# Kernel optimization log

Measured on AMD Instinct MI355X. Metric: run time of the kernel, lower is better.

The kernel has to match this reference:

```python
import jax, jax.numpy as jnp
import numpy as np

H, DK, DV, SEG, D = 16, 64, 64, 512, 1024


def setup_inputs() -> dict:
    key = jax.random.key(0)
    ks = jax.random.split(key, 6)
    B, T = 2, 8192
    x = jax.random.normal(ks[0], (B, T, D), jnp.float32)
    Wq = jax.random.normal(ks[1], (H * DK, D), jnp.float32) * 0.02
    Wk = jax.random.normal(ks[2], (H * DK, D), jnp.float32) * 0.02
    Wv = jax.random.normal(ks[3], (H * DV, D), jnp.float32) * 0.02
    Wout = jax.random.normal(ks[4], (D, H * DV), jnp.float32) * 0.02
    betas = jax.random.normal(ks[5], (1, H, 1, DV), jnp.float32)
    return {"x": x, "Wq": Wq, "Wk": Wk, "Wv": Wv, "Wout": Wout, "betas": betas}


def reference(x, Wq, Wk, Wv, Wout, betas):
    B, T, _ = x.shape
    n_seg = T // SEG
    # Projections for the whole sequence, then PyTorch-style .view head split:
    # per segment, (B, SEG, H*dk).view(B, H, SEG, dk) is a raw row-major reshape.
    q = (x @ Wq.T).reshape(B, n_seg, H, SEG, DK)
    k = (x @ Wk.T).reshape(B, n_seg, H, SEG, DK)
    v = (x @ Wv.T).reshape(B, n_seg, H, SEG, DV)
    qs = jnp.moveaxis(q, 1, 0)  # (n_seg, B, H, SEG, DK)
    ks_ = jnp.moveaxis(k, 1, 0)
    vs = jnp.moveaxis(v, 1, 0)

    gate = jax.nn.sigmoid(betas)                 # (1, H, 1, DV)
    scale = 1.0 / jnp.sqrt(jnp.float32(DK))

    mem0 = jnp.zeros((B, H, DK, DV), x.dtype)
    # z broadcasts from (B,H,DV,1) to (B,H,DV,DK) on first update; start dense.
    z0 = jnp.zeros((B, H, DV, DK), x.dtype)

    def step(carry, seg):
        mem, z = carry
        q, k, v = seg
        sq = jax.nn.elu(q) + 1.0                 # (B,H,S,DK)
        sk = jax.nn.elu(k) + 1.0
        z = z + sk.sum(axis=-2, keepdims=True)   # (B,H,DV,DK) via broadcast
        scores = jnp.einsum('bhsd,bhtd->bhst', q, k) * scale
        att_dot = jnp.einsum('bhst,bhtv->bhsv', jax.nn.softmax(scores, axis=-1), v)
        att_mem = jnp.einsum('bhsd,bhdv->bhsv', sq, mem) / jnp.einsum('bhsd,bhdv->bhsv', sq, z)
        mem = mem + jnp.einsum('bhsd,bhsv->bhdv', sk, v)  # linear update (after att_mem)
        att = gate * att_mem + (1.0 - gate) * att_dot     # (B,H,S,DV)
        # PyTorch .view(B, SEG, H*DV) on (B,H,S,DV): raw reshape, no transpose.
        y = att.reshape(B, SEG, H * DV) @ Wout.T          # (B,SEG,D)
        return (mem, z), y

    (_, _), ys = jax.lax.scan(step, (mem0, z0), (qs, ks_, vs))
    out = jnp.moveaxis(ys, 0, 1).reshape(B, T, D)
    return out
```

## Files before the change

### kernel.cpp

```cpp
#include <hip/hip_runtime.h>


#define H_ 16
#define SEG_ 512
#define NSEG_ 16
#define B_ 2
#define T_ 8192
#define D_ 1024
#define BT_ 16384

#define NPROJ ((size_t)BT_ * D_)
#define NW ((size_t)D_ * D_)

__device__ unsigned short g_qb[NPROJ], g_kb[NPROJ], g_vb[NPROJ];
__device__ unsigned short g_xh[NPROJ];
__device__ unsigned short g_wqkv[3 * NW];
__device__ unsigned short g_ath[NPROJ], g_atl[NPROJ];
__device__ unsigned short g_woh[NW], g_wol[NW];
__device__ unsigned short g_vt[(size_t)512 * 64 * 512];
__device__ float g_M[(size_t)512 * 4096];
__device__ float g_z[(size_t)512 * 64];

typedef __attribute__((ext_vector_type(8))) short short8;
typedef __attribute__((ext_vector_type(8))) unsigned short ushort8;
typedef __attribute__((ext_vector_type(4))) float f32x4;

__device__ __forceinline__ float elu1(float x) {
    return x > 0.f ? x + 1.f : __expf(x);
}
__device__ __forceinline__ unsigned short f2bf(float x) {
    unsigned u = __float_as_uint(x);
    u += 0x7fffu + ((u >> 16) & 1u);
    return (unsigned short)(u >> 16);
}
__device__ __forceinline__ float bf2f(unsigned short h) {
    return __uint_as_float((unsigned)h << 16);
}
__device__ __forceinline__ void load_lds16(const unsigned short* g, unsigned short* l) {
    __builtin_amdgcn_global_load_lds(
        (const __attribute__((address_space(1))) unsigned int*)g,
        (__attribute__((address_space(3))) unsigned int*)l, 16, 0, 0);
}

__global__ __launch_bounds__(256) void cast_bf16(
    const float* __restrict__ in, unsigned short* __restrict__ out, int n)
{
    int i = (blockIdx.x * 256 + threadIdx.x) * 4;
    if (i >= n) return;
    float4 x = *(const float4*)(in + i);
    ushort4 h;
    h.x = f2bf(x.x); h.y = f2bf(x.y); h.z = f2bf(x.z); h.w = f2bf(x.w);
    *(ushort4*)(out + i) = h;
}

__global__ __launch_bounds__(256) void split_bf16(
    const float* __restrict__ in, unsigned short* __restrict__ hi,
    unsigned short* __restrict__ lo, int n)
{
    int i = (blockIdx.x * 256 + threadIdx.x) * 4;
    if (i >= n) return;
    float4 x = *(const float4*)(in + i);
    ushort4 h, l;
    h.x = f2bf(x.x); l.x = f2bf(x.x - bf2f(h.x));
    h.y = f2bf(x.y); l.y = f2bf(x.y - bf2f(h.y));
    h.z = f2bf(x.z); l.z = f2bf(x.z - bf2f(h.z));
    h.w = f2bf(x.w); l.w = f2bf(x.w - bf2f(h.w));
    *(ushort4*)(hi + i) = h;
    *(ushort4*)(lo + i) = l;
}


#define VMC(N) asm volatile("s_waitcnt vmcnt(" #N ")" ::: "memory")

#define STAGE_A(p, h, tt, u) \
    load_lds16(Aw + ((h) * 128 + (u) * 8) * 1024 + (tt) * 64, \
               &lds[(p) * 32768 + ((h) * 128 + w * 16 + (u) * 8) * 64])
#define STAGE_B(p, h, tt, u) \
    load_lds16(Bww + ((h) * 128 + (u) * 8) * 1024 + (tt) * 64, \
               &lds[(p) * 32768 + 16384 + ((h) * 128 + w * 16 + (u) * 8) * 64])
#define STAGE_AH(p, h, tt) do { STAGE_A(p, h, tt, 0); STAGE_A(p, h, tt, 1); } while (0)
#define STAGE_BH(p, h, tt) do { STAGE_B(p, h, tt, 0); STAGE_B(p, h, tt, 1); } while (0)

#define LDA(PBUF, MLO) do { \
    _Pragma("unroll") for (int m2 = 0; m2 < 4; ++m2) \
    _Pragma("unroll") for (int ks2 = 0; ks2 < 2; ++ks2) \
        a[m2][ks2] = *(const short8*)&lds[(PBUF) * 32768 + aoff[ks2] + ((MLO) + m2) * 1024]; \
} while (0)

#define LDB(PBUF) do { \
    _Pragma("unroll") for (int n2 = 0; n2 < 4; ++n2) \
    _Pragma("unroll") for (int ks2 = 0; ks2 < 2; ++ks2) \
        b[n2][ks2] = *(const short8*)&lds[(PBUF) * 32768 + boff[ks2] + n2 * 1024]; \
} while (0)

#define MFMA_QUAD(MLO, NLO) do { \
    _Pragma("unroll") for (int m2 = 0; m2 < 4; ++m2) \
    _Pragma("unroll") for (int n2 = 0; n2 < 2; ++n2) \
    _Pragma("unroll") for (int ks2 = 0; ks2 < 2; ++ks2) \
        acc[(MLO) + m2][(NLO) + n2] = __builtin_amdgcn_mfma_f32_16x16x32_bf16( \
            a[m2][ks2], b[(NLO) + n2][ks2], acc[(MLO) + m2][(NLO) + n2], 0, 0, 0); \
} while (0)

#define PH(MLO, NLO) do { \
    __builtin_amdgcn_s_barrier(); \
    asm volatile("s_waitcnt lgkmcnt(0)" ::: "memory"); \
    __builtin_amdgcn_sched_barrier(0); \
    __builtin_amdgcn_s_setprio(1); \
    MFMA_QUAD(MLO, NLO); \
    __builtin_amdgcn_s_setprio(0); \
    __builtin_amdgcn_sched_barrier(0); \
    __builtin_amdgcn_s_barrier(); \
} while (0)

__global__ __launch_bounds__(512, 2) void gemm_qkv8(
    const unsigned short* __restrict__ A, const unsigned short* __restrict__ Bw,
    unsigned short* __restrict__ Q, unsigned short* __restrict__ Kp,
    unsigned short* __restrict__ V)
{
    __shared__ unsigned short lds[65536];
    const int t = threadIdx.x, lane = t & 63, w = t >> 6;
    const int wave_m = w >> 2, wave_n = w & 3;

    const int bid = blockIdx.x;
    const int sb = (bid & 7) * 96 + (bid >> 3);
    const int mb = sb / 12, nb = sb % 12;
    const int m0 = mb * 256, n0 = nb * 256;

    const int lrow = lane >> 3;
    const int lcol = ((lane & 7) ^ lrow) * 8;
    const unsigned short* Aw  = A  + (size_t)(m0 + w * 16 + lrow) * 1024 + lcol;
    const unsigned short* Bww = Bw + (size_t)(n0 + w * 16 + lrow) * 1024 + lcol;

    const int fr = lane & 15, g4 = lane >> 4;
    int aoff[2], boff[2];
#pragma unroll
    for (int ks2 = 0; ks2 < 2; ++ks2) {
        aoff[ks2] = (wave_m * 128 + fr) * 64 + (((ks2 * 4 + g4) ^ (fr & 7)) * 8);
        boff[ks2] = 16384 + (wave_n * 64 + fr) * 64 + (((ks2 * 4 + g4) ^ (fr & 7)) * 8);
    }

    f32x4 acc[8][4];
#pragma unroll
    for (int i = 0; i < 8; ++i)
#pragma unroll
        for (int j = 0; j < 4; ++j) acc[i][j] = (f32x4)0.f;
    short8 a[4][2], b[4][2];

    STAGE_BH(0, 0, 0); STAGE_BH(0, 1, 0); STAGE_AH(0, 0, 0); STAGE_AH(0, 1, 0);
    STAGE_BH(1, 0, 1); STAGE_BH(1, 1, 1); STAGE_AH(1, 0, 1);
    VMC(6);
    __builtin_amdgcn_s_barrier();

#pragma unroll 1
    for (int it = 0; it < 7; ++it) {
        const int t1 = 2 * it + 1, t2 = 2 * it + 2, t3 = 2 * it + 3;
        LDB(0); LDA(0, 0);
        STAGE_AH(1, 1, t1);
        PH(0, 0);
        STAGE_BH(0, 0, t2);
        PH(0, 2);
        LDA(0, 4);
        STAGE_BH(0, 1, t2);
        PH(4, 0);
        STAGE_AH(0, 0, t2);
        VMC(6);
        PH(4, 2);
        LDB(1); LDA(1, 0);
        STAGE_AH(0, 1, t2);
        PH(0, 0);
        STAGE_BH(1, 0, t3);
        PH(0, 2);
        LDA(1, 4);
        STAGE_BH(1, 1, t3);
        PH(4, 0);
        STAGE_AH(1, 0, t3);
        VMC(6);
        PH(4, 2);
    }
    LDB(0); LDA(0, 0);
    STAGE_AH(1, 1, 15);
    PH(0, 0);
    PH(0, 2);
    LDA(0, 4);
    PH(4, 0);
    VMC(0);
    PH(4, 2);
    LDB(1); LDA(1, 0);
    PH(0, 0);
    PH(0, 2);
    LDA(1, 4);
    PH(4, 0);
    PH(4, 2);

    const int ccol = lane & 15, crow = (lane >> 4) * 4;
#pragma unroll
    for (int m = 0; m < 8; ++m)
#pragma unroll
        for (int n = 0; n < 4; ++n) {
            const int row = wave_m * 128 + m * 16 + crow;
            const int col = wave_n * 64 + n * 16 + ccol;
#pragma unroll
            for (int r = 0; r < 4; ++r)
                lds[(row + r) * 256 + col] = f2bf(acc[m][n][r]);
        }
    __syncthreads();
    const int which = n0 >> 10, col0 = n0 & 1023;
    unsigned short* outp = which == 0 ? Q : (which == 1 ? Kp : V);
    const int orow = t >> 1, och = (t & 1) * 128;
    unsigned short* gp = outp + (size_t)(m0 + orow) * 1024 + col0 + och;
    const unsigned short* lp = &lds[orow * 256 + och];
#pragma unroll
    for (int u = 0; u < 128; u += 8)
        *(ushort8*)(gp + u) = *(const ushort8*)(lp + u);
}


#define OSTG(p, arrp, aroff, tt, u) \
    load_lds16(arrp + (size_t)(u) * 16 * 1024 + (tt) * 32, \
               &lds[(p) * 32768 + (aroff) + (w * 32 + (u) * 16) * 32])
#define OUNIT(p, arrp, aroff, tt) do { OSTG(p, arrp, aroff, tt, 0); OSTG(p, arrp, aroff, tt, 1); } while (0)

#define OLDA(PBUF, MLO) do { \
    _Pragma("unroll") for (int m2 = 0; m2 < 4; ++m2) { \
        ah[m2] = *(const short8*)&lds[(PBUF) * 32768 +         ao + ((MLO) + m2) * 512]; \
        al[m2] = *(const short8*)&lds[(PBUF) * 32768 +  8192 + ao + ((MLO) + m2) * 512]; \
    } \
} while (0)

#define OLDB(PBUF) do { \
    _Pragma("unroll") for (int n2 = 0; n2 < 4; ++n2) { \
        bh[n2] = *(const short8*)&lds[(PBUF) * 32768 + 16384 + bo + n2 * 512]; \
        bl[n2] = *(const short8*)&lds[(PBUF) * 32768 + 24576 + bo + n2 * 512]; \
    } \
} while (0)

#define OQUAD(MLO, NLO) do { \
    _Pragma("unroll") for (int m2 = 0; m2 < 4; ++m2) \
    _Pragma("unroll") for (int n2 = 0; n2 < 2; ++n2) { \
        acc[(MLO) + m2][(NLO) + n2] = __builtin_amdgcn_mfma_f32_16x16x32_bf16( \
            ah[m2], bh[(NLO) + n2], acc[(MLO) + m2][(NLO) + n2], 0, 0, 0); \
        acc[(MLO) + m2][(NLO) + n2] = __builtin_amdgcn_mfma_f32_16x16x32_bf16( \
            al[m2], bh[(NLO) + n2], acc[(MLO) + m2][(NLO) + n2], 0, 0, 0); \
        acc[(MLO) + m2][(NLO) + n2] = __builtin_amdgcn_mfma_f32_16x16x32_bf16( \
            ah[m2], bl[(NLO) + n2], acc[(MLO) + m2][(NLO) + n2], 0, 0, 0); \
    } \
} while (0)

#define OPH(MLO, NLO) do { \
    __builtin_amdgcn_s_barrier(); \
    asm volatile("s_waitcnt lgkmcnt(0)" ::: "memory"); \
    __builtin_amdgcn_sched_barrier(0); \
    __builtin_amdgcn_s_setprio(1); \
    OQUAD(MLO, NLO); \
    __builtin_amdgcn_s_setprio(0); \
    __builtin_amdgcn_sched_barrier(0); \
    __builtin_amdgcn_s_barrier(); \
} while (0)

__global__ __launch_bounds__(512, 2) void gemm_bt8(
    const unsigned short* __restrict__ Ah, const unsigned short* __restrict__ Al,
    const unsigned short* __restrict__ Bh, const unsigned short* __restrict__ Bl,
    float* __restrict__ C)
{
    __shared__ unsigned short lds[65536];
    const int t = threadIdx.x, lane = t & 63, w = t >> 6;
    const int wave_m = w >> 2, wave_n = w & 3;

    const int bid = blockIdx.x;
    const int sb = (bid & 7) * 32 + (bid >> 3);
    const int m0 = (sb >> 2) * 256, n0 = (sb & 3) * 256;

    const int lrow = lane >> 2;
    const int lcol = ((lane & 3) ^ ((lane >> 3) & 3)) * 8;
    const unsigned short* Ahp = Ah + (size_t)(m0 + w * 32 + lrow) * 1024 + lcol;
    const unsigned short* Alp = Al + (size_t)(m0 + w * 32 + lrow) * 1024 + lcol;
    const unsigned short* Bhp = Bh + (size_t)(n0 + w * 32 + lrow) * 1024 + lcol;
    const unsigned short* Blp = Bl + (size_t)(n0 + w * 32 + lrow) * 1024 + lcol;

    const int fr = lane & 15, g4 = lane >> 4;
    const int xo = (g4 ^ ((fr >> 1) & 3)) * 8;
    const int ao = (wave_m * 128 + fr) * 32 + xo;
    const int bo = (wave_n * 64 + fr) * 32 + xo;

    f32x4 acc[8][4];
#pragma unroll
    for (int i = 0; i < 8; ++i)
#pragma unroll
        for (int j = 0; j < 4; ++j) acc[i][j] = (f32x4)0.f;
    short8 ah[4], al[4], bh[4], bl[4];

    OUNIT(0, Bhp, 16384, 0); OUNIT(0, Blp, 24576, 0); OUNIT(0, Ahp, 0, 0); OUNIT(0, Alp, 8192, 0);
    OUNIT(1, Bhp, 16384, 1); OUNIT(1, Blp, 24576, 1); OUNIT(1, Ahp, 0, 1);
    VMC(6);
    __builtin_amdgcn_s_barrier();

#pragma unroll 1
    for (int it = 0; it < 15; ++it) {
        const int t1 = 2 * it + 1, t2 = 2 * it + 2, t3 = 2 * it + 3;
        OLDB(0); OLDA(0, 0);
        OUNIT(1, Alp, 8192, t1);
        OPH(0, 0);
        OUNIT(0, Bhp, 16384, t2);
        OPH(0, 2);
        OLDA(0, 4);
        OUNIT(0, Blp, 24576, t2);
        OPH(4, 0);
        OUNIT(0, Ahp, 0, t2);
        VMC(6);
        OPH(4, 2);
        OLDB(1); OLDA(1, 0);
        OUNIT(0, Alp, 8192, t2);
        OPH(0, 0);
        OUNIT(1, Bhp, 16384, t3);
        OPH(0, 2);
        OLDA(1, 4);
        OUNIT(1, Blp, 24576, t3);
        OPH(4, 0);
        OUNIT(1, Ahp, 0, t3);
        VMC(6);
        OPH(4, 2);
    }
    OLDB(0); OLDA(0, 0);
    OUNIT(1, Alp, 8192, 31);
    OPH(0, 0);
    OPH(0, 2);
    OLDA(0, 4);
    OPH(4, 0);
    VMC(0);
    OPH(4, 2);
    OLDB(1); OLDA(1, 0);
    OPH(0, 0);
    OPH(0, 2);
    OLDA(1, 4);
    OPH(4, 0);
    OPH(4, 2);

    const int ccol = lane & 15, crow = (lane >> 4) * 4;
#pragma unroll
    for (int m = 0; m < 8; ++m)
#pragma unroll
        for (int n = 0; n < 4; ++n) {
            float* cp = C + (size_t)(m0 + wave_m * 128 + m * 16 + crow) * 1024
                          + (n0 + wave_n * 64 + n * 16 + ccol);
#pragma unroll
            for (int r = 0; r < 4; ++r) cp[(size_t)r * 1024] = acc[m][n][r];
        }
}

__global__ __launch_bounds__(256) void seg_stats(
    const unsigned short* __restrict__ kproj, const unsigned short* __restrict__ vproj,
    float* __restrict__ Mseg, float* __restrict__ zsum,
    unsigned short* __restrict__ vtg)
{
    __shared__ float ks[64][68];
    __shared__ float vs[64][68];
    const int idx = blockIdx.x;
    const int seg = idx & 15;
    const int bh  = idx >> 4;
    const int h   = bh & 15;
    const int b   = bh >> 4;
    const size_t base = ((size_t)b * T_ + (size_t)seg * SEG_ + (size_t)h * 32) * D_;
    const unsigned short* kt = kproj + base;
    const unsigned short* vt = vproj + base;
    const int t  = threadIdx.x;
    const int d0 = (t >> 4) * 4;
    const int v0 = (t & 15) * 4;
    const int lr = t >> 2;
    const int lc = (t & 3) * 16;
    float acc[4][4];
#pragma unroll
    for (int i = 0; i < 4; ++i)
#pragma unroll
        for (int j = 0; j < 4; ++j) acc[i][j] = 0.f;
    float zacc = 0.f;

    for (int c0 = 0; c0 < SEG_; c0 += 64) {
        __syncthreads();
        {
            const unsigned short* kp = kt + (size_t)(c0 + lr) * 64 + lc;
            const unsigned short* vp = vt + (size_t)(c0 + lr) * 64 + lc;
            ushort8 k0 = *(const ushort8*)kp,       k1 = *(const ushort8*)(kp + 8);
            ushort8 v0v = *(const ushort8*)vp,      v1 = *(const ushort8*)(vp + 8);
#pragma unroll
            for (int e = 0; e < 8; ++e) {
                ks[lr][lc + e]     = elu1(bf2f(k0[e]));
                ks[lr][lc + 8 + e] = elu1(bf2f(k1[e]));
                vs[lr][lc + e]     = bf2f(v0v[e]);
                vs[lr][lc + 8 + e] = bf2f(v1[e]);
            }
        }
        __syncthreads();
#pragma unroll 8
        for (int i = 0; i < 64; ++i) {
            float a0 = ks[i][d0 + 0], a1 = ks[i][d0 + 1];
            float a2 = ks[i][d0 + 2], a3 = ks[i][d0 + 3];
            float b0 = vs[i][v0 + 0], b1 = vs[i][v0 + 1];
            float b2 = vs[i][v0 + 2], b3 = vs[i][v0 + 3];
            acc[0][0] += a0 * b0; acc[0][1] += a0 * b1; acc[0][2] += a0 * b2; acc[0][3] += a0 * b3;
            acc[1][0] += a1 * b0; acc[1][1] += a1 * b1; acc[1][2] += a1 * b2; acc[1][3] += a1 * b3;
            acc[2][0] += a2 * b0; acc[2][1] += a2 * b1; acc[2][2] += a2 * b2; acc[2][3] += a2 * b3;
            acc[3][0] += a3 * b0; acc[3][1] += a3 * b1; acc[3][2] += a3 * b2; acc[3][3] += a3 * b3;
        }
        if (t < 64) {
#pragma unroll 8
            for (int i = 0; i < 64; ++i) zacc += ks[i][t];
        }
        {
            ushort8 w0, w1;
#pragma unroll
            for (int i = 0; i < 8; ++i) w0[i] = f2bf(vs[lc + i][lr]);
#pragma unroll
            for (int i = 0; i < 8; ++i) w1[i] = f2bf(vs[lc + 8 + i][lr]);
            unsigned short* vo = vtg + ((size_t)idx * 64 + lr) * 512 + c0 + lc;
            *(ushort8*)vo       = w0;
            *(ushort8*)(vo + 8) = w1;
        }
    }
    float* Mout = Mseg + (size_t)idx * 4096;
#pragma unroll
    for (int i = 0; i < 4; ++i)
        *(float4*)(Mout + (size_t)(d0 + i) * 64 + v0) =
            make_float4(acc[i][0], acc[i][1], acc[i][2], acc[i][3]);
    if (t < 64) zsum[(size_t)idx * 64 + t] = zacc;
}

__global__ __launch_bounds__(256) void prefix_scan(
    float* __restrict__ M, float* __restrict__ z)
{
    const int bh = blockIdx.x;
    const int t  = threadIdx.x;
    float run[16];
#pragma unroll
    for (int u = 0; u < 16; ++u) run[u] = 0.f;
    float runz = 0.f;
    for (int seg = 0; seg < NSEG_; ++seg) {
        const size_t o = ((size_t)bh * NSEG_ + seg) * 4096 + (size_t)t * 16;
#pragma unroll
        for (int u = 0; u < 16; u += 4) {
            float4 m = *(const float4*)(M + o + u);
            *(float4*)(M + o + u) = make_float4(run[u], run[u+1], run[u+2], run[u+3]);
            run[u] += m.x; run[u+1] += m.y; run[u+2] += m.z; run[u+3] += m.w;
        }
        if (t < 64) {
            const size_t oz = ((size_t)bh * NSEG_ + seg) * 64 + t;
            runz += z[oz];
            z[oz] = runz;
        }
    }
}

__global__ __launch_bounds__(256) void attn_mfma(
    const unsigned short* __restrict__ qproj, const unsigned short* __restrict__ kproj,
    const unsigned short* __restrict__ vtg, const float* __restrict__ memb,
    const float* __restrict__ Zaf, const float* __restrict__ betas,
    unsigned short* __restrict__ ath, unsigned short* __restrict__ atl)
{
    __shared__ unsigned short sm_k[64 * 72];
    __shared__ unsigned short sm_v[64 * 72];
    __shared__ unsigned short sm_p[64 * 72];
    __shared__ float Zsh[64], gsh[64];

    const int idx  = blockIdx.x;
    const int qc   = idx & 7;
    const int rest = idx >> 3;
    const int seg  = rest & 15;
    const int bh   = rest >> 4;
    const int h    = bh & 15;
    const int b    = bh >> 4;
    const size_t base = ((size_t)b * T_ + (size_t)seg * SEG_ + (size_t)h * 32) * D_;

    const int t    = threadIdx.x;
    const int lane = t & 63;
    const int w    = t >> 6;
    const int c16  = lane & 15;
    const int g4   = lane >> 4;
    const int lr   = t >> 2;
    const int lc   = (t & 3) * 16;

    const unsigned short* qt = qproj + base + (size_t)qc * 4096;
    const unsigned short* kt = kproj + base;
    const unsigned short* vt = vtg + (size_t)rest * (64 * 512);
    const float* mb = memb + (size_t)rest * 4096;

    if (t < 64) {
        Zsh[t] = Zaf[(size_t)rest * 64 + t];
        gsh[t] = 1.f / (1.f + __expf(-betas[h * 64 + t]));
    }

    short8 qh[2], sqh[2];
    float rowsum = 0.f;
#pragma unroll
    for (int ks = 0; ks < 2; ++ks) {
        const unsigned short* qp = qt + (size_t)(w * 16 + c16) * 64 + g4 * 8 + ks * 32;
        ushort8 qv = *(const ushort8*)qp;
        short8 qf, sf;
#pragma unroll
        for (int j = 0; j < 8; ++j) {
            float e = elu1(bf2f(qv[j]));
            rowsum += e;
            qf[j] = (short)qv[j];
            sf[j] = (short)f2bf(e);
        }
        qh[ks] = qf; sqh[ks] = sf;
    }
    rowsum += __shfl_xor(rowsum, 16);
    rowsum += __shfl_xor(rowsum, 32);

    {
        const float* mp = mb + (size_t)lr * 64 + lc;
#pragma unroll
        for (int u = 0; u < 4; ++u) {
            float4 m4 = *(const float4*)(mp + u * 4);
            sm_p[(lc + u * 4 + 0) * 72 + lr] = f2bf(m4.x);
            sm_p[(lc + u * 4 + 1) * 72 + lr] = f2bf(m4.y);
            sm_p[(lc + u * 4 + 2) * 72 + lr] = f2bf(m4.z);
            sm_p[(lc + u * 4 + 3) * 72 + lr] = f2bf(m4.w);
        }
    }
    __syncthreads();

    f32x4 numf[4];
#pragma unroll
    for (int nf = 0; nf < 4; ++nf) numf[nf] = (f32x4)0.f;
#pragma unroll
    for (int ks = 0; ks < 2; ++ks)
#pragma unroll
        for (int nf = 0; nf < 4; ++nf) {
            short8 bm = *(const short8*)&sm_p[(nf * 16 + c16) * 72 + g4 * 8 + ks * 32];
            numf[nf] = __builtin_amdgcn_mfma_f32_16x16x32_bf16(sqh[ks], bm, numf[nf], 0, 0, 0);
        }

    f32x4 o[4];
#pragma unroll
    for (int nf = 0; nf < 4; ++nf) o[nf] = (f32x4)0.f;
    float mrow[4] = {-1e30f, -1e30f, -1e30f, -1e30f};
    float lrow[4] = {0.f, 0.f, 0.f, 0.f};

    for (int kb = 0; kb < 8; ++kb) {
        __syncthreads();
        {
            const unsigned short* kp = kt + (size_t)(kb * 64 + lr) * 64 + lc;
            *(ushort8*)&sm_k[lr * 72 + lc]     = *(const ushort8*)kp;
            *(ushort8*)&sm_k[lr * 72 + lc + 8] = *(const ushort8*)(kp + 8);
            const unsigned short* vp = vt + (size_t)lr * 512 + kb * 64 + lc;
            *(ushort8*)&sm_v[lr * 72 + lc]     = *(const ushort8*)vp;
            *(ushort8*)&sm_v[lr * 72 + lc + 8] = *(const ushort8*)(vp + 8);
        }
        __syncthreads();

        f32x4 s[4];
#pragma unroll
        for (int nf = 0; nf < 4; ++nf) s[nf] = (f32x4)0.f;
#pragma unroll
        for (int ks = 0; ks < 2; ++ks)
#pragma unroll
            for (int nf = 0; nf < 4; ++nf) {
                short8 bk = *(const short8*)&sm_k[(nf * 16 + c16) * 72 + g4 * 8 + ks * 32];
                s[nf] = __builtin_amdgcn_mfma_f32_16x16x32_bf16(qh[ks], bk, s[nf], 0, 0, 0);
            }
#pragma unroll
        for (int nf = 0; nf < 4; ++nf) s[nf] *= 0.125f;

        float corr[4];
#pragma unroll
        for (int r = 0; r < 4; ++r) {
            float mx = fmaxf(fmaxf(s[0][r], s[1][r]), fmaxf(s[2][r], s[3][r]));
            mx = fmaxf(mx, __shfl_xor(mx, 1));
            mx = fmaxf(mx, __shfl_xor(mx, 2));
            mx = fmaxf(mx, __shfl_xor(mx, 4));
            mx = fmaxf(mx, __shfl_xor(mx, 8));
            float mnew = fmaxf(mrow[r], mx);
            corr[r] = __expf(mrow[r] - mnew);
            mrow[r] = mnew;
        }
#pragma unroll
        for (int nf = 0; nf < 4; ++nf)
#pragma unroll
            for (int r = 0; r < 4; ++r)
                s[nf][r] = __expf(s[nf][r] - mrow[r]);
#pragma unroll
        for (int r = 0; r < 4; ++r) {
            float ps = s[0][r] + s[1][r] + s[2][r] + s[3][r];
            ps += __shfl_xor(ps, 1);
            ps += __shfl_xor(ps, 2);
            ps += __shfl_xor(ps, 4);
            ps += __shfl_xor(ps, 8);
            lrow[r] = lrow[r] * corr[r] + ps;
        }
#pragma unroll
        for (int nf = 0; nf < 4; ++nf)
#pragma unroll
            for (int r = 0; r < 4; ++r) o[nf][r] *= corr[r];

#pragma unroll
        for (int nf = 0; nf < 4; ++nf)
#pragma unroll
            for (int r = 0; r < 4; ++r)
                sm_p[(w * 16 + g4 * 4 + r) * 72 + nf * 16 + c16] = f2bf(s[nf][r]);

#pragma unroll
        for (int ks = 0; ks < 2; ++ks) {
            short8 pa = *(const short8*)&sm_p[(w * 16 + c16) * 72 + g4 * 8 + ks * 32];
#pragma unroll
            for (int nf = 0; nf < 4; ++nf) {
                short8 bv = *(const short8*)&sm_v[(nf * 16 + c16) * 72 + g4 * 8 + ks * 32];
                o[nf] = __builtin_amdgcn_mfma_f32_16x16x32_bf16(pa, bv, o[nf], 0, 0, 0);
            }
        }
    }

    __syncthreads();

    float rs[4], invl[4];
#pragma unroll
    for (int r = 0; r < 4; ++r) {
        rs[r]   = __shfl(rowsum, (g4 << 2) + r);
        invl[r] = 1.f / lrow[r];
    }
#pragma unroll
    for (int nf = 0; nf < 4; ++nf) {
        const int col = nf * 16 + c16;
        const float Zc = Zsh[col], gc = gsh[col];
        const float izc = 1.f / Zc;
#pragma unroll
        for (int r = 0; r < 4; ++r) {
            const float adot = o[nf][r] * invl[r];
            const float amem = numf[nf][r] * izc / rs[r];
            const float res  = gc * amem + (1.f - gc) * adot;
            const unsigned short hv = f2bf(res);
            const unsigned short lv = f2bf(res - bf2f(hv));
            const int row = w * 16 + g4 * 4 + r;
            sm_k[row * 72 + col] = hv;
            sm_v[row * 72 + col] = lv;
        }
    }
    __syncthreads();
    {
        const size_t ob = base + (size_t)(qc * 64 + lr) * 64 + lc;
        *(ushort8*)(ath + ob)     = *(const ushort8*)&sm_k[lr * 72 + lc];
        *(ushort8*)(ath + ob + 8) = *(const ushort8*)&sm_k[lr * 72 + lc + 8];
        *(ushort8*)(atl + ob)     = *(const ushort8*)&sm_v[lr * 72 + lc];
        *(ushort8*)(atl + ob + 8) = *(const ushort8*)&sm_v[lr * 72 + lc + 8];
    }
}

extern "C" void kernel_launch(void* const* d_in, const int* in_sizes, int n_in,
                              void* d_out, int out_size, void* d_ws, size_t ws_size,
                              hipStream_t stream) {
    const float* x     = (const float*)d_in[0];
    const float* Wq    = (const float*)d_in[1];
    const float* Wk    = (const float*)d_in[2];
    const float* Wv    = (const float*)d_in[3];
    const float* Wout  = (const float*)d_in[4];
    const float* betas = (const float*)d_in[5];
    float* out = (float*)d_out;
    (void)d_ws; (void)ws_size;

    float *M, *z;
    unsigned short *qb, *kb, *vb, *xh, *wqkv, *vt, *ath, *atl, *woh, *wol;
    hipGetSymbolAddress((void**)&qb,   HIP_SYMBOL(g_qb));
    hipGetSymbolAddress((void**)&kb,   HIP_SYMBOL(g_kb));
    hipGetSymbolAddress((void**)&vb,   HIP_SYMBOL(g_vb));
    hipGetSymbolAddress((void**)&xh,   HIP_SYMBOL(g_xh));
    hipGetSymbolAddress((void**)&wqkv, HIP_SYMBOL(g_wqkv));
    hipGetSymbolAddress((void**)&vt,   HIP_SYMBOL(g_vt));
    hipGetSymbolAddress((void**)&ath,  HIP_SYMBOL(g_ath));
    hipGetSymbolAddress((void**)&atl,  HIP_SYMBOL(g_atl));
    hipGetSymbolAddress((void**)&woh,  HIP_SYMBOL(g_woh));
    hipGetSymbolAddress((void**)&wol,  HIP_SYMBOL(g_wol));
    hipGetSymbolAddress((void**)&M,    HIP_SYMBOL(g_M));
    hipGetSymbolAddress((void**)&z,    HIP_SYMBOL(g_z));

    const int nX = (int)NPROJ, nW = (int)NW;
    cast_bf16<<<nX / 1024, 256, 0, stream>>>(x, xh, nX);
    cast_bf16<<<nW / 1024, 256, 0, stream>>>(Wq, wqkv, nW);
    cast_bf16<<<nW / 1024, 256, 0, stream>>>(Wk, wqkv + NW, nW);
    cast_bf16<<<nW / 1024, 256, 0, stream>>>(Wv, wqkv + 2 * NW, nW);
    split_bf16<<<nW / 1024, 256, 0, stream>>>(Wout, woh, wol, nW);

    gemm_qkv8<<<dim3(768), 512, 0, stream>>>(xh, wqkv, qb, kb, vb);
    seg_stats<<<B_ * H_ * NSEG_, 256, 0, stream>>>(kb, vb, M, z, vt);
    prefix_scan<<<B_ * H_, 256, 0, stream>>>(M, z);
    attn_mfma<<<B_ * H_ * NSEG_ * 8, 256, 0, stream>>>(qb, kb, vt, M, z, betas, ath, atl);
    gemm_bt8<<<dim3(256), 512, 0, stream>>>(ath, atl, woh, wol, out);
}
```

Measured before the change: 559.6 us.

## Swizzle attention LDS tiles, lazy softmax rescale, MFMA row sums, remap blocks

Replaces the padded 72-stride LDS tiles in the attention kernel with an XOR-swizzled 64-stride layout to avoid bank conflicts while using less shared memory. The online softmax now rescales only when some row max exceeds the running max by more than 8, skipping the shuffle reductions and output rescaling in most iterations. Row sums of P are computed with an extra MFMA against a ones vector instead of shuffles. The block index mapping is also reordered so neighbouring blocks share different (b,h,seg) tiles. The lazy threshold relies on exp staying bounded in fp32/bf16.

```diff
diff --git a/kernel.cpp b/kernel.cpp
--- a/kernel.cpp
+++ b/kernel.cpp
@@ -40,6 +40,9 @@
     __builtin_amdgcn_global_load_lds(
         (const __attribute__((address_space(1))) unsigned int*)g,
         (__attribute__((address_space(3))) unsigned int*)l, 16, 0, 0);
+}
+__device__ __forceinline__ int sz8(int row, int blk) {
+    return row * 64 + ((blk ^ (row & 7)) << 3);
 }
 
 __global__ __launch_bounds__(256) void cast_bf16(
@@ -455,16 +458,16 @@
     const float* __restrict__ Zaf, const float* __restrict__ betas,
     unsigned short* __restrict__ ath, unsigned short* __restrict__ atl)
 {
-    __shared__ unsigned short sm_k[64 * 72];
-    __shared__ unsigned short sm_v[64 * 72];
-    __shared__ unsigned short sm_p[64 * 72];
+    __shared__ unsigned short sm_k[64 * 64];
+    __shared__ unsigned short sm_v[64 * 64];
+    __shared__ unsigned short sm_p[64 * 64];
     __shared__ float Zsh[64], gsh[64];
 
     const int idx  = blockIdx.x;
-    const int qc   = idx & 7;
-    const int rest = idx >> 3;
+    const int qc   = (idx >> 3) & 7;
+    const int rest = (idx >> 6) * 8 + (idx & 7);
+    const int bh   = rest >> 4;
     const int seg  = rest & 15;
-    const int bh   = rest >> 4;
     const int h    = bh & 15;
     const int b    = bh >> 4;
     const size_t base = ((size_t)b * T_ + (size_t)seg * SEG_ + (size_t)h * 32) * D_;
@@ -511,10 +514,10 @@
 #pragma unroll
         for (int u = 0; u < 4; ++u) {
             float4 m4 = *(const float4*)(mp + u * 4);
-            sm_p[(lc + u * 4 + 0) * 72 + lr] = f2bf(m4.x);
-            sm_p[(lc + u * 4 + 1) * 72 + lr] = f2bf(m4.y);
-            sm_p[(lc + u * 4 + 2) * 72 + lr] = f2bf(m4.z);
-            sm_p[(lc + u * 4 + 3) * 72 + lr] = f2bf(m4.w);
+            sm_p[sz8(lc + u * 4 + 0, lr >> 3) + (lr & 7)] = f2bf(m4.x);
+            sm_p[sz8(lc + u * 4 + 1, lr >> 3) + (lr & 7)] = f2bf(m4.y);
+            sm_p[sz8(lc + u * 4 + 2, lr >> 3) + (lr & 7)] = f2bf(m4.z);
+            sm_p[sz8(lc + u * 4 + 3, lr >> 3) + (lr & 7)] = f2bf(m4.w);
         }
     }
     __syncthreads();
@@ -526,9 +529,13 @@
     for (int ks = 0; ks < 2; ++ks)
 #pragma unroll
         for (int nf = 0; nf < 4; ++nf) {
-            short8 bm = *(const short8*)&sm_p[(nf * 16 + c16) * 72 + g4 * 8 + ks * 32];
+            short8 bm = *(const short8*)&sm_p[sz8(nf * 16 + c16, g4 + ks * 4)];
             numf[nf] = __builtin_amdgcn_mfma_f32_16x16x32_bf16(sqh[ks], bm, numf[nf], 0, 0, 0);
         }
+
+    short8 bones;
+#pragma unroll
+    for (int j = 0; j < 8; ++j) bones[j] = (short)0x3F80;
 
     f32x4 o[4];
 #pragma unroll
@@ -540,11 +547,11 @@
         __syncthreads();
         {
             const unsigned short* kp = kt + (size_t)(kb * 64 + lr) * 64 + lc;
-            *(ushort8*)&sm_k[lr * 72 + lc]     = *(const ushort8*)kp;
-            *(ushort8*)&sm_k[lr * 72 + lc + 8] = *(const ushort8*)(kp + 8);
+            *(ushort8*)&sm_k[sz8(lr, lc >> 3)]       = *(const ushort8*)kp;
+            *(ushort8*)&sm_k[sz8(lr, (lc >> 3) + 1)] = *(const ushort8*)(kp + 8);
             const unsigned short* vp = vt + (size_t)lr * 512 + kb * 64 + lc;
-            *(ushort8*)&sm_v[lr * 72 + lc]     = *(const ushort8*)vp;
-            *(ushort8*)&sm_v[lr * 72 + lc + 8] = *(const ushort8*)(vp + 8);
+            *(ushort8*)&sm_v[sz8(lr, lc >> 3)]       = *(const ushort8*)vp;
+            *(ushort8*)&sm_v[sz8(lr, (lc >> 3) + 1)] = *(const ushort8*)(vp + 8);
         }
         __syncthreads();
 
@@ -555,58 +562,56 @@
         for (int ks = 0; ks < 2; ++ks)
 #pragma unroll
             for (int nf = 0; nf < 4; ++nf) {
-                short8 bk = *(const short8*)&sm_k[(nf * 16 + c16) * 72 + g4 * 8 + ks * 32];
+                short8 bk = *(const short8*)&sm_k[sz8(nf * 16 + c16, g4 + ks * 4)];
                 s[nf] = __builtin_amdgcn_mfma_f32_16x16x32_bf16(qh[ks], bk, s[nf], 0, 0, 0);
             }
 #pragma unroll
         for (int nf = 0; nf < 4; ++nf) s[nf] *= 0.125f;
 
-        float corr[4];
-#pragma unroll
-        for (int r = 0; r < 4; ++r) {
-            float mx = fmaxf(fmaxf(s[0][r], s[1][r]), fmaxf(s[2][r], s[3][r]));
-            mx = fmaxf(mx, __shfl_xor(mx, 1));
-            mx = fmaxf(mx, __shfl_xor(mx, 2));
-            mx = fmaxf(mx, __shfl_xor(mx, 4));
-            mx = fmaxf(mx, __shfl_xor(mx, 8));
-            float mnew = fmaxf(mrow[r], mx);
-            corr[r] = __expf(mrow[r] - mnew);
-            mrow[r] = mnew;
+        float pmax[4];
+#pragma unroll
+        for (int r = 0; r < 4; ++r)
+            pmax[r] = fmaxf(fmaxf(s[0][r], s[1][r]), fmaxf(s[2][r], s[3][r]));
+        const bool ok = pmax[0] <= mrow[0] + 8.f && pmax[1] <= mrow[1] + 8.f &&
+                        pmax[2] <= mrow[2] + 8.f && pmax[3] <= mrow[3] + 8.f;
+        if (!__all(ok)) {
+#pragma unroll
+            for (int r = 0; r < 4; ++r) {
+                float mx = pmax[r];
+                mx = fmaxf(mx, __shfl_xor(mx, 1));
+                mx = fmaxf(mx, __shfl_xor(mx, 2));
+                mx = fmaxf(mx, __shfl_xor(mx, 4));
+                mx = fmaxf(mx, __shfl_xor(mx, 8));
+                const float mnew = fmaxf(mrow[r], mx);
+                const float corr = __expf(mrow[r] - mnew);
+                mrow[r] = mnew;
+                lrow[r] *= corr;
+#pragma unroll
+                for (int nf = 0; nf < 4; ++nf) o[nf][r] *= corr;
+            }
         }
 #pragma unroll
         for (int nf = 0; nf < 4; ++nf)
 #pragma unroll
-            for (int r = 0; r < 4; ++r)
+            for (int r = 0; r < 4; ++r) {
                 s[nf][r] = __expf(s[nf][r] - mrow[r]);
-#pragma unroll
-        for (int r = 0; r < 4; ++r) {
-            float ps = s[0][r] + s[1][r] + s[2][r] + s[3][r];
-            ps += __shfl_xor(ps, 1);
-            ps += __shfl_xor(ps, 2);
-            ps += __shfl_xor(ps, 4);
-            ps += __shfl_xor(ps, 8);
-            lrow[r] = lrow[r] * corr[r] + ps;
-        }
-#pragma unroll
-        for (int nf = 0; nf < 4; ++nf)
-#pragma unroll
-            for (int r = 0; r < 4; ++r) o[nf][r] *= corr[r];
-
-#pragma unroll
-        for (int nf = 0; nf < 4; ++nf)
-#pragma unroll
-            for (int r = 0; r < 4; ++r)
-                sm_p[(w * 16 + g4 * 4 + r) * 72 + nf * 16 + c16] = f2bf(s[nf][r]);
-
+                sm_p[sz8(w * 16 + g4 * 4 + r, nf * 2 + (c16 >> 3)) + (c16 & 7)] =
+                    f2bf(s[nf][r]);
+            }
+
+        f32x4 psum = (f32x4)0.f;
 #pragma unroll
         for (int ks = 0; ks < 2; ++ks) {
-            short8 pa = *(const short8*)&sm_p[(w * 16 + c16) * 72 + g4 * 8 + ks * 32];
+            short8 pa = *(const short8*)&sm_p[sz8(w * 16 + c16, g4 + ks * 4)];
+            psum = __builtin_amdgcn_mfma_f32_16x16x32_bf16(pa, bones, psum, 0, 0, 0);
 #pragma unroll
             for (int nf = 0; nf < 4; ++nf) {
-                short8 bv = *(const short8*)&sm_v[(nf * 16 + c16) * 72 + g4 * 8 + ks * 32];
+                short8 bv = *(const short8*)&sm_v[sz8(nf * 16 + c16, g4 + ks * 4)];
                 o[nf] = __builtin_amdgcn_mfma_f32_16x16x32_bf16(pa, bv, o[nf], 0, 0, 0);
             }
         }
+#pragma unroll
+        for (int r = 0; r < 4; ++r) lrow[r] += psum[r];
     }
 
     __syncthreads();
@@ -630,17 +635,18 @@
             const unsigned short hv = f2bf(res);
             const unsigned short lv = f2bf(res - bf2f(hv));
             const int row = w * 16 + g4 * 4 + r;
-            sm_k[row * 72 + col] = hv;
-            sm_v[row * 72 + col] = lv;
+            const int so  = sz8(row, nf * 2 + (c16 >> 3)) + (c16 & 7);
+            sm_k[so] = hv;
+            sm_v[so] = lv;
         }
     }
     __syncthreads();
     {
         const size_t ob = base + (size_t)(qc * 64 + lr) * 64 + lc;
-        *(ushort8*)(ath + ob)     = *(const ushort8*)&sm_k[lr * 72 + lc];
-        *(ushort8*)(ath + ob + 8) = *(const ushort8*)&sm_k[lr * 72 + lc + 8];
-        *(ushort8*)(atl + ob)     = *(const ushort8*)&sm_v[lr * 72 + lc];
-        *(ushort8*)(atl + ob + 8) = *(const ushort8*)&sm_v[lr * 72 + lc + 8];
+        *(ushort8*)(ath + ob)     = *(const ushort8*)&sm_k[sz8(lr, lc >> 3)];
+        *(ushort8*)(ath + ob + 8) = *(const ushort8*)&sm_k[sz8(lr, (lc >> 3) + 1)];
+        *(ushort8*)(atl + ob)     = *(const ushort8*)&sm_v[sz8(lr, lc >> 3)];
+        *(ushort8*)(atl + ob + 8) = *(const ushort8*)&sm_v[sz8(lr, (lc >> 3) + 1)];
     }
 }
 
```

New measurement: 512.2 us. 8.5% less time.
